# Kernel tuning notes

Measured on AMD Instinct MI355X. Metric: run time of the kernel, lower is better.

Reference implementation:

```python
import jax, jax.numpy as jnp
import numpy as np

N_NODES = 100000
N_EDGES = 800000
D = 128
BN_EPS = 1e-5


def setup_inputs() -> dict:
    key = jax.random.key(0)
    k1, k2, k3 = jax.random.split(key, 3)
    x = jax.random.normal(k1, (N_NODES, D), dtype=jnp.float32)
    # Glorot-ish init for the GCN weight
    W = jax.random.normal(k2, (D, D), dtype=jnp.float32) * (1.0 / np.sqrt(D))
    b = jnp.zeros((D,), dtype=jnp.float32)
    gamma = jnp.ones((D,), dtype=jnp.float32)
    beta = jnp.zeros((D,), dtype=jnp.float32)
    edge_index = jax.random.randint(k3, (2, N_EDGES), 0, N_NODES, dtype=jnp.int64)
    return {"x": x, "W": W, "b": b, "gamma": gamma, "beta": beta,
            "edge_index": edge_index}


def reference(x, W, b, gamma, beta, edge_index):
    N = x.shape[0]
    # --- GCNConv: add self-loops, symmetric degree normalization ---
    loop = jnp.arange(N, dtype=edge_index.dtype)
    src = jnp.concatenate([edge_index[0], loop])
    dst = jnp.concatenate([edge_index[1], loop])
    deg = jax.ops.segment_sum(jnp.ones_like(dst, dtype=x.dtype), dst,
                              num_segments=N)
    deg_inv_sqrt = jax.lax.rsqrt(deg)  # deg >= 1 thanks to self-loops
    norm = deg_inv_sqrt[src] * deg_inv_sqrt[dst]  # [E+N]

    h = x @ W  # [N, D] linear transform before propagation
    msg = h[src] * norm[:, None]  # gather + edge scaling, [E+N, D]
    agg = jax.ops.segment_sum(msg, dst, num_segments=N) + b  # scatter-add

    # --- BatchNorm1d (training-mode batch statistics, biased variance) ---
    mean = jnp.mean(agg, axis=0)
    var = jnp.mean(jnp.square(agg - mean), axis=0)
    y = gamma * (agg - mean) * jax.lax.rsqrt(var + BN_EPS) + beta

    # --- ReLU (dropout is identity in deterministic reference) ---
    return jax.nn.relu(y)
```

## Files before the change

kernel.cpp:

```cpp
#include <hip/hip_runtime.h>


#define N_NODES 100000
#define N_EDGES 800000
#define D 128
#define BN_EPS 1e-5f
#define SCAN_NB 98

__global__ void detect_i64(const unsigned int* ei, int* flag) {
    __shared__ int nonzero;
    if (threadIdx.x == 0) nonzero = 0;
    __syncthreads();
    int local = 0;
    for (int i = threadIdx.x; i < 2048; i += 256)
        if (ei[2 * i + 1] != 0u) local = 1;
    if (local) atomicOr(&nonzero, 1);
    __syncthreads();
    if (threadIdx.x == 0) *flag = (nonzero == 0) ? 1 : 0;
}

__device__ __forceinline__ int edge_at(const void* ei, int is64, long long pos) {
    if (is64) return (int)((const long long*)ei)[pos];
    return ((const int*)ei)[pos];
}

__global__ void count_deg_i(const void* ei, const int* __restrict__ flag,
                            int* __restrict__ deg) {
    int is64 = *flag;
    for (int i = blockIdx.x * blockDim.x + threadIdx.x; i < N_EDGES;
         i += gridDim.x * blockDim.x) {
        int d = edge_at(ei, is64, (long long)N_EDGES + i);
        atomicAdd(&deg[d], 1);
    }
}

__global__ __launch_bounds__(256) void scan1(const int* __restrict__ deg,
                                             int* __restrict__ rp,
                                             int* __restrict__ bsum) {
    __shared__ int wsum[4];
    int tid = threadIdx.x;
    int base = blockIdx.x * 1024;
    int v[4];
#pragma unroll
    for (int i = 0; i < 4; ++i) {
        int idx = base + tid * 4 + i;
        v[i] = (idx < N_NODES) ? deg[idx] : 0;
    }
    int tsum = v[0] + v[1] + v[2] + v[3];
    int lane = tid & 63;
    int incl = tsum;
#pragma unroll
    for (int off = 1; off < 64; off <<= 1) {
        int n = __shfl_up(incl, off, 64);
        if (lane >= off) incl += n;
    }
    int wid = tid >> 6;
    if (lane == 63) wsum[wid] = incl;
    __syncthreads();
    int woff = 0;
    for (int w = 0; w < wid; ++w) woff += wsum[w];
    int run = woff + incl - tsum;
#pragma unroll
    for (int i = 0; i < 4; ++i) {
        int idx = base + tid * 4 + i;
        if (idx < N_NODES) rp[idx] = run;
        run += v[i];
    }
    if (tid == 255) bsum[blockIdx.x] = woff + incl;
}

__global__ void scan2(int* __restrict__ bsum, int* __restrict__ rp) {
    __shared__ int s[128];
    int t = threadIdx.x;
    if (t < SCAN_NB) s[t] = bsum[t];
    __syncthreads();
    if (t == 0) {
        int run = 0;
        for (int i = 0; i < SCAN_NB; ++i) { int x = s[i]; s[i] = run; run += x; }
        rp[N_NODES] = N_EDGES;
    }
    __syncthreads();
    if (t < SCAN_NB) bsum[t] = s[t];
}

__global__ void scan3(int* __restrict__ rp, const int* __restrict__ bsum,
                      int* __restrict__ fp, const int* __restrict__ deg,
                      float* __restrict__ dis) {
    int idx = blockIdx.x * 256 + threadIdx.x;
    if (idx < N_NODES) {
        int v = rp[idx] + bsum[idx >> 10];
        rp[idx] = v;
        fp[idx] = v;
        dis[idx] = rsqrtf((float)deg[idx] + 1.0f);
    }
}

__global__ void fill_csr(const void* ei, const int* __restrict__ flag,
                         int* __restrict__ fp, const float* __restrict__ dis,
                         int2* __restrict__ eb) {
    int is64 = *flag;
    for (int e = blockIdx.x * blockDim.x + threadIdx.x; e < N_EDGES;
         e += gridDim.x * blockDim.x) {
        int s = edge_at(ei, is64, e);
        int d = edge_at(ei, is64, (long long)N_EDGES + e);
        float coef = dis[s] * dis[d];
        int pos = atomicAdd(&fp[d], 1);
        eb[pos] = make_int2(s, __float_as_int(coef));
    }
}

__global__ __launch_bounds__(256) void gather_x(const int* __restrict__ rp,
                                                const int2* __restrict__ eb,
                                                const float* __restrict__ dis,
                                                const float* __restrict__ x,
                                                float* __restrict__ aggx) {
    int lane = threadIdx.x & 63;
    int wid = threadIdx.x >> 6;
    const float2* x2 = (const float2*)x;
    for (int node = blockIdx.x * 4 + wid; node < N_NODES;
         node += gridDim.x * 4) {
        int beg = rp[node], end = rp[node + 1];
        float dd = dis[node];
        float2 xv = x2[(size_t)node * 64 + lane];
        float c2 = dd * dd;
        float a0 = xv.x * c2, a1 = xv.y * c2;
        int j = beg;
        for (; j + 4 <= end; j += 4) {
            int2 e0 = eb[j], e1 = eb[j + 1], e2 = eb[j + 2], e3 = eb[j + 3];
            float2 v0 = x2[(size_t)e0.x * 64 + lane];
            float2 v1 = x2[(size_t)e1.x * 64 + lane];
            float2 v2 = x2[(size_t)e2.x * 64 + lane];
            float2 v3 = x2[(size_t)e3.x * 64 + lane];
            float c0 = __int_as_float(e0.y), c1 = __int_as_float(e1.y);
            float cc = __int_as_float(e2.y), c3 = __int_as_float(e3.y);
            a0 = fmaf(v0.x, c0, a0); a1 = fmaf(v0.y, c0, a1);
            a0 = fmaf(v1.x, c1, a0); a1 = fmaf(v1.y, c1, a1);
            a0 = fmaf(v2.x, cc, a0); a1 = fmaf(v2.y, cc, a1);
            a0 = fmaf(v3.x, c3, a0); a1 = fmaf(v3.y, c3, a1);
        }
        for (; j < end; ++j) {
            int2 e = eb[j];
            float2 v = x2[(size_t)e.x * 64 + lane];
            float c = __int_as_float(e.y);
            a0 = fmaf(v.x, c, a0); a1 = fmaf(v.y, c, a1);
        }
        ((float2*)aggx)[(size_t)node * 64 + lane] = make_float2(a0, a1);
    }
}

__global__ __launch_bounds__(256) void gemm_stats(float* __restrict__ ax,
                                                  const float* __restrict__ Wm,
                                                  float* __restrict__ colsum,
                                                  float* __restrict__ colsumsq) {
    __shared__ float red[8 * 128];
    int tid = threadIdx.x;
    int row0 = blockIdx.x * 64;
    int tx = tid & 31;
    int ty = tid >> 5;

    const float4* W4 = (const float4*)Wm;

    const float4* arow[8];
    float rmask[8];
#pragma unroll
    for (int r = 0; r < 8; ++r) {
        int gr = row0 + ty * 8 + r;
        int cg = (gr < N_NODES) ? gr : 0;
        arow[r] = (const float4*)(ax + (size_t)cg * 128);
        rmask[r] = (gr < N_NODES) ? 1.0f : 0.0f;
    }

    float acc[8][4] = {};

    for (int kc = 0; kc < 32; ++kc) {
        float4 a8[8];
#pragma unroll
        for (int r = 0; r < 8; ++r) a8[r] = arow[r][kc];
        float4 w[4];
#pragma unroll
        for (int kk = 0; kk < 4; ++kk) w[kk] = W4[(kc * 4 + kk) * 32 + tx];
#pragma unroll
        for (int kk = 0; kk < 4; ++kk) {
#pragma unroll
            for (int r = 0; r < 8; ++r) {
                float av = (kk == 0) ? a8[r].x : (kk == 1) ? a8[r].y
                         : (kk == 2) ? a8[r].z : a8[r].w;
                acc[r][0] = fmaf(av, w[kk].x, acc[r][0]);
                acc[r][1] = fmaf(av, w[kk].y, acc[r][1]);
                acc[r][2] = fmaf(av, w[kk].z, acc[r][2]);
                acc[r][3] = fmaf(av, w[kk].w, acc[r][3]);
            }
        }
    }

#pragma unroll
    for (int r = 0; r < 8; ++r) {
        int gr = row0 + ty * 8 + r;
        if (gr < N_NODES)
            ((float4*)&ax[(size_t)gr * 128])[tx] =
                make_float4(acc[r][0], acc[r][1], acc[r][2], acc[r][3]);
    }

    float ps[4] = {0.f, 0.f, 0.f, 0.f}, pq[4] = {0.f, 0.f, 0.f, 0.f};
#pragma unroll
    for (int r = 0; r < 8; ++r)
#pragma unroll
        for (int k = 0; k < 4; ++k) {
            float v = acc[r][k] * rmask[r];
            ps[k] += v;
            pq[k] += v * v;
        }
#pragma unroll
    for (int k = 0; k < 4; ++k) {
        ps[k] += __shfl_xor(ps[k], 32);
        pq[k] += __shfl_xor(pq[k], 32);
    }
    int wv = tid >> 6;
    if ((tid & 32) == 0) {
#pragma unroll
        for (int k = 0; k < 4; ++k) {
            red[wv * 128 + tx * 4 + k] = ps[k];
            red[(4 + wv) * 128 + tx * 4 + k] = pq[k];
        }
    }
    __syncthreads();
    if (tid < 128) {
        float s = 0.f, q = 0.f;
#pragma unroll
        for (int w = 0; w < 4; ++w) {
            s += red[w * 128 + tid];
            q += red[(4 + w) * 128 + tid];
        }
        atomicAdd(&colsum[tid], s);
        atomicAdd(&colsumsq[tid], q);
    }
}

__global__ void finalize_bn(const float* __restrict__ colsum,
                            const float* __restrict__ colsumsq,
                            const float* __restrict__ gamma,
                            const float* __restrict__ beta,
                            float* __restrict__ scale, float* __restrict__ shift) {
    int c = threadIdx.x;
    float mean = colsum[c] * (1.0f / N_NODES);
    float var = colsumsq[c] * (1.0f / N_NODES) - mean * mean;
    float sc = gamma[c] * rsqrtf(var + BN_EPS);
    scale[c] = sc;
    shift[c] = beta[c] - mean * sc;
}

__global__ __launch_bounds__(256) void normalize_relu(float* __restrict__ out,
                                                      const float* __restrict__ scale,
                                                      const float* __restrict__ shift) {
    const int total = N_NODES * 32;
    float4* o4 = (float4*)out;
    const float4* sc4 = (const float4*)scale;
    const float4* sh4 = (const float4*)shift;
    for (int i = blockIdx.x * blockDim.x + threadIdx.x; i < total;
         i += gridDim.x * blockDim.x) {
        int cg = i & 31;
        float4 v = o4[i];
        float4 sc = sc4[cg];
        float4 sh = sh4[cg];
        v.x = fmaxf(fmaf(v.x, sc.x, sh.x), 0.f);
        v.y = fmaxf(fmaf(v.y, sc.y, sh.y), 0.f);
        v.z = fmaxf(fmaf(v.z, sc.z, sh.z), 0.f);
        v.w = fmaxf(fmaf(v.w, sc.w, sh.w), 0.f);
        o4[i] = v;
    }
}

extern "C" void kernel_launch(void* const* d_in, const int* in_sizes, int n_in,
                              void* d_out, int out_size, void* d_ws, size_t ws_size,
                              hipStream_t stream) {
    const float* x = (const float*)d_in[0];
    const float* Wm = (const float*)d_in[1];
    const float* gamma = (const float*)d_in[3];
    const float* beta = (const float*)d_in[4];
    const void* ei = d_in[5];

    float* out = (float*)d_out;

    int2* eb = (int2*)d_ws;
    int* deg = (int*)(eb + N_EDGES);
    int* rp = deg + N_NODES;
    int* fp = rp + N_NODES + 1;
    int* bsum = fp + N_NODES;
    float* dis = (float*)(bsum + 128);
    float* colsum = dis + N_NODES;
    float* colsumsq = colsum + 128;
    float* scale = colsumsq + 128;
    float* shift = scale + 128;
    int* flag = (int*)(shift + 128);

    hipMemsetAsync(deg, 0, (size_t)N_NODES * sizeof(int), stream);
    hipMemsetAsync(colsum, 0, 256 * sizeof(float), stream);

    detect_i64<<<1, 256, 0, stream>>>((const unsigned int*)ei, flag);
    count_deg_i<<<2048, 256, 0, stream>>>(ei, flag, deg);
    scan1<<<SCAN_NB, 256, 0, stream>>>(deg, rp, bsum);
    scan2<<<1, 128, 0, stream>>>(bsum, rp);
    scan3<<<(N_NODES + 255) / 256, 256, 0, stream>>>(rp, bsum, fp, deg, dis);
    fill_csr<<<2048, 256, 0, stream>>>(ei, flag, fp, dis, eb);
    gather_x<<<2048, 256, 0, stream>>>(rp, eb, dis, x, out);
    gemm_stats<<<(N_NODES + 63) / 64, 256, 0, stream>>>(out, Wm, colsum, colsumsq);
    finalize_bn<<<1, 128, 0, stream>>>(colsum, colsumsq, gamma, beta, scale, shift);
    normalize_relu<<<2048, 256, 0, stream>>>(out, scale, shift);
}
```

Measured before the change: 400.3 us.

## Stage GEMM tiles into LDS with async global_load_lds double buffering

```diff
diff --git a/kernel.cpp b/kernel.cpp
--- a/kernel.cpp
+++ b/kernel.cpp
@@ -6,6 +6,13 @@
 #define D 128
 #define BN_EPS 1e-5f
 #define SCAN_NB 98
+
+typedef const __attribute__((address_space(1))) void* gas_ptr;
+typedef __attribute__((address_space(3))) void* las_ptr;
+
+__device__ __forceinline__ void gload16(const float* g, void* l) {
+    __builtin_amdgcn_global_load_lds((gas_ptr)(const void*)g, (las_ptr)l, 16, 0, 0);
+}
 
 __global__ void detect_i64(const unsigned int* ei, int* flag) {
     __shared__ int nonzero;
@@ -152,45 +159,66 @@
                                                   const float* __restrict__ Wm,
                                                   float* __restrict__ colsum,
                                                   float* __restrict__ colsumsq) {
-    __shared__ float red[8 * 128];
+    __shared__ float Abuf[2][64 * 32];
+    __shared__ float Wbuf[2][32 * 128];
     int tid = threadIdx.x;
-    int row0 = blockIdx.x * 64;
     int tx = tid & 31;
     int ty = tid >> 5;
-
-    const float4* W4 = (const float4*)Wm;
-
-    const float4* arow[8];
-    float rmask[8];
-#pragma unroll
-    for (int r = 0; r < 8; ++r) {
-        int gr = row0 + ty * 8 + r;
-        int cg = (gr < N_NODES) ? gr : 0;
-        arow[r] = (const float4*)(ax + (size_t)cg * 128);
-        rmask[r] = (gr < N_NODES) ? 1.0f : 0.0f;
-    }
+    int wid = tid >> 6;
+    int lane = tid & 63;
+    int row0 = blockIdx.x * 64;
+
+    auto stage = [&](int b, int kc) {
+#pragma unroll
+        for (int i = 0; i < 2; ++i) {
+            int seg = wid * 2 + i;
+            int idx = seg * 64 + lane;
+            int row = idx >> 3, c4 = idx & 7;
+            int gr = row0 + row;
+            if (gr >= N_NODES) gr = N_NODES - 1;
+            const float* src = ax + (size_t)gr * 128 + kc + c4 * 4;
+            gload16(src, (char*)&Abuf[b][0] + seg * 1024);
+        }
+#pragma unroll
+        for (int i = 0; i < 4; ++i) {
+            int seg = wid * 4 + i;
+            int idx = seg * 64 + lane;
+            const float* src = Wm + (size_t)kc * 128 + (size_t)idx * 4;
+            gload16(src, (char*)&Wbuf[b][0] + seg * 1024);
+        }
+    };
+
+    stage(0, 0);
+    __syncthreads();
 
     float acc[8][4] = {};
 
-    for (int kc = 0; kc < 32; ++kc) {
-        float4 a8[8];
-#pragma unroll
-        for (int r = 0; r < 8; ++r) a8[r] = arow[r][kc];
-        float4 w[4];
-#pragma unroll
-        for (int kk = 0; kk < 4; ++kk) w[kk] = W4[(kc * 4 + kk) * 32 + tx];
-#pragma unroll
-        for (int kk = 0; kk < 4; ++kk) {
-#pragma unroll
-            for (int r = 0; r < 8; ++r) {
-                float av = (kk == 0) ? a8[r].x : (kk == 1) ? a8[r].y
-                         : (kk == 2) ? a8[r].z : a8[r].w;
-                acc[r][0] = fmaf(av, w[kk].x, acc[r][0]);
-                acc[r][1] = fmaf(av, w[kk].y, acc[r][1]);
-                acc[r][2] = fmaf(av, w[kk].z, acc[r][2]);
-                acc[r][3] = fmaf(av, w[kk].w, acc[r][3]);
+#pragma unroll 1
+    for (int t = 0; t < 4; ++t) {
+        if (t < 3) stage((t + 1) & 1, (t + 1) * 32);
+        asm volatile("" ::: "memory");
+        const float4* As4 = (const float4*)Abuf[t & 1];
+        const float4* Ws4 = (const float4*)Wbuf[t & 1];
+        for (int k4 = 0; k4 < 32; k4 += 4) {
+            float4 a8[8];
+#pragma unroll
+            for (int r = 0; r < 8; ++r)
+                a8[r] = As4[(ty * 8 + r) * 8 + (k4 >> 2)];
+#pragma unroll
+            for (int kk = 0; kk < 4; ++kk) {
+                float4 w = Ws4[(k4 + kk) * 32 + tx];
+#pragma unroll
+                for (int r = 0; r < 8; ++r) {
+                    float av = (kk == 0) ? a8[r].x : (kk == 1) ? a8[r].y
+                             : (kk == 2) ? a8[r].z : a8[r].w;
+                    acc[r][0] = fmaf(av, w.x, acc[r][0]);
+                    acc[r][1] = fmaf(av, w.y, acc[r][1]);
+                    acc[r][2] = fmaf(av, w.z, acc[r][2]);
+                    acc[r][3] = fmaf(av, w.w, acc[r][3]);
+                }
             }
         }
+        __syncthreads();
     }
 
 #pragma unroll
@@ -203,24 +231,27 @@
 
     float ps[4] = {0.f, 0.f, 0.f, 0.f}, pq[4] = {0.f, 0.f, 0.f, 0.f};
 #pragma unroll
-    for (int r = 0; r < 8; ++r)
+    for (int r = 0; r < 8; ++r) {
+        int gr = row0 + ty * 8 + r;
+        float m = (gr < N_NODES) ? 1.0f : 0.0f;
 #pragma unroll
         for (int k = 0; k < 4; ++k) {
-            float v = acc[r][k] * rmask[r];
+            float v = acc[r][k] * m;
             ps[k] += v;
             pq[k] += v * v;
         }
+    }
 #pragma unroll
     for (int k = 0; k < 4; ++k) {
         ps[k] += __shfl_xor(ps[k], 32);
         pq[k] += __shfl_xor(pq[k], 32);
     }
-    int wv = tid >> 6;
+    float* red = (float*)Abuf;
     if ((tid & 32) == 0) {
 #pragma unroll
         for (int k = 0; k < 4; ++k) {
-            red[wv * 128 + tx * 4 + k] = ps[k];
-            red[(4 + wv) * 128 + tx * 4 + k] = pq[k];
+            red[wid * 128 + tx * 4 + k] = ps[k];
+            red[1024 + wid * 128 + tx * 4 + k] = pq[k];
         }
     }
     __syncthreads();
@@ -229,7 +260,7 @@
 #pragma unroll
         for (int w = 0; w < 4; ++w) {
             s += red[w * 128 + tid];
-            q += red[(4 + w) * 128 + tid];
+            q += red[1024 + w * 128 + tid];
         }
         atomicAdd(&colsum[tid], s);
         atomicAdd(&colsumsq[tid], q);
```

After: 355.8 us. -11.1%, faster.

## Replace FP32 FMA GEMM with split-bf16 MFMA GEMM fused with column stats

Applied to the files above, without the earlier changes.

```diff
diff --git a/kernel.cpp b/kernel.cpp
--- a/kernel.cpp
+++ b/kernel.cpp
@@ -6,6 +6,18 @@
 #define D 128
 #define BN_EPS 1e-5f
 #define SCAN_NB 98
+
+using bf16x8 = __attribute__((ext_vector_type(8))) short;
+using f32x4 = __attribute__((ext_vector_type(4))) float;
+
+__device__ __forceinline__ unsigned short f2b(float f) {
+    unsigned u = __float_as_uint(f);
+    unsigned r = ((u >> 16) & 1u) + 0x7fffu;
+    return (unsigned short)((u + r) >> 16);
+}
+__device__ __forceinline__ float b2f(unsigned short h) {
+    return __uint_as_float(((unsigned)h) << 16);
+}
 
 __global__ void detect_i64(const unsigned int* ei, int* flag) {
     __shared__ int nonzero;
@@ -109,11 +121,33 @@
     }
 }
 
+__global__ void prep_w(const float* __restrict__ Wm, bf16x8* __restrict__ Whi,
+                       bf16x8* __restrict__ Wlo) {
+    for (int slot = threadIdx.x; slot < 2048; slot += 256) {
+        int t = slot >> 9;
+        int rem = slot & 511;
+        int c = rem >> 6;
+        int l = rem & 63;
+        int k0 = t * 32 + ((l >> 4) << 3);
+        int col = c * 16 + (l & 15);
+        bf16x8 hi, lo;
+#pragma unroll
+        for (int j = 0; j < 8; ++j) {
+            float v = Wm[(size_t)(k0 + j) * 128 + col];
+            unsigned short h = f2b(v);
+            hi[j] = (short)h;
+            lo[j] = (short)f2b(v - b2f(h));
+        }
+        Whi[slot] = hi;
+        Wlo[slot] = lo;
+    }
+}
+
 __global__ __launch_bounds__(256) void gather_x(const int* __restrict__ rp,
                                                 const int2* __restrict__ eb,
                                                 const float* __restrict__ dis,
                                                 const float* __restrict__ x,
-                                                float* __restrict__ aggx) {
+                                                void* __restrict__ aggx) {
     int lane = threadIdx.x & 63;
     int wid = threadIdx.x >> 6;
     const float2* x2 = (const float2*)x;
@@ -144,93 +178,68 @@
             float c = __int_as_float(e.y);
             a0 = fmaf(v.x, c, a0); a1 = fmaf(v.y, c, a1);
         }
-        ((float2*)aggx)[(size_t)node * 64 + lane] = make_float2(a0, a1);
-    }
-}
-
-__global__ __launch_bounds__(256) void gemm_stats(float* __restrict__ ax,
-                                                  const float* __restrict__ Wm,
-                                                  float* __restrict__ colsum,
-                                                  float* __restrict__ colsumsq) {
-    __shared__ float red[8 * 128];
+        unsigned short h0 = f2b(a0), h1 = f2b(a1);
+        unsigned short q0 = f2b(a0 - b2f(h0)), q1 = f2b(a1 - b2f(h1));
+        ushort2* rowp = (ushort2*)((char*)aggx + (size_t)node * 512);
+        rowp[lane] = make_ushort2(h0, h1);
+        rowp[64 + lane] = make_ushort2(q0, q1);
+    }
+}
+
+__global__ __launch_bounds__(256) void gemm_mfma(float* __restrict__ out,
+                                                 const bf16x8* __restrict__ Whi,
+                                                 const bf16x8* __restrict__ Wlo,
+                                                 float* __restrict__ colsum,
+                                                 float* __restrict__ colsumsq) {
+    __shared__ float sps[4][128], spq[4][128];
     int tid = threadIdx.x;
+    int w = tid >> 6;
+    int l = tid & 63;
     int row0 = blockIdx.x * 64;
-    int tx = tid & 31;
-    int ty = tid >> 5;
-
-    const float4* W4 = (const float4*)Wm;
-
-    const float4* arow[8];
-    float rmask[8];
-#pragma unroll
-    for (int r = 0; r < 8; ++r) {
-        int gr = row0 + ty * 8 + r;
-        int cg = (gr < N_NODES) ? gr : 0;
-        arow[r] = (const float4*)(ax + (size_t)cg * 128);
-        rmask[r] = (gr < N_NODES) ? 1.0f : 0.0f;
-    }
-
-    float acc[8][4] = {};
-
-    for (int kc = 0; kc < 32; ++kc) {
-        float4 a8[8];
-#pragma unroll
-        for (int r = 0; r < 8; ++r) a8[r] = arow[r][kc];
-        float4 w[4];
-#pragma unroll
-        for (int kk = 0; kk < 4; ++kk) w[kk] = W4[(kc * 4 + kk) * 32 + tx];
-#pragma unroll
-        for (int kk = 0; kk < 4; ++kk) {
-#pragma unroll
-            for (int r = 0; r < 8; ++r) {
-                float av = (kk == 0) ? a8[r].x : (kk == 1) ? a8[r].y
-                         : (kk == 2) ? a8[r].z : a8[r].w;
-                acc[r][0] = fmaf(av, w[kk].x, acc[r][0]);
-                acc[r][1] = fmaf(av, w[kk].y, acc[r][1]);
-                acc[r][2] = fmaf(av, w[kk].z, acc[r][2]);
-                acc[r][3] = fmaf(av, w[kk].w, acc[r][3]);
+
+    int arow = row0 + w * 16 + (l & 15);
+    if (arow >= N_NODES) arow = N_NODES - 1;
+    const char* abase = (const char*)out + (size_t)arow * 512;
+    int ao = (l >> 4) << 4;
+    bf16x8 ahi[4], alo[4];
+#pragma unroll
+    for (int t = 0; t < 4; ++t) {
+        ahi[t] = *(const bf16x8*)(abase + t * 64 + ao);
+        alo[t] = *(const bf16x8*)(abase + 256 + t * 64 + ao);
+    }
+
+    int rbase = row0 + w * 16 + ((l >> 4) << 2);
+#pragma unroll
+    for (int c = 0; c < 8; ++c) {
+        f32x4 acc = {0.f, 0.f, 0.f, 0.f};
+#pragma unroll
+        for (int t = 0; t < 4; ++t) {
+            bf16x8 bh = Whi[(t * 8 + c) * 64 + l];
+            bf16x8 bl = Wlo[(t * 8 + c) * 64 + l];
+            acc = __builtin_amdgcn_mfma_f32_16x16x32_bf16(ahi[t], bh, acc, 0, 0, 0);
+            acc = __builtin_amdgcn_mfma_f32_16x16x32_bf16(alo[t], bh, acc, 0, 0, 0);
+            acc = __builtin_amdgcn_mfma_f32_16x16x32_bf16(ahi[t], bl, acc, 0, 0, 0);
+        }
+        int col = c * 16 + (l & 15);
+        float ps = 0.f, pq = 0.f;
+#pragma unroll
+        for (int j = 0; j < 4; ++j) {
+            int orow = rbase + j;
+            float v = acc[j];
+            if (orow < N_NODES) {
+                out[(size_t)orow * 128 + col] = v;
+                ps += v;
+                pq += v * v;
             }
         }
-    }
-
-#pragma unroll
-    for (int r = 0; r < 8; ++r) {
-        int gr = row0 + ty * 8 + r;
-        if (gr < N_NODES)
-            ((float4*)&ax[(size_t)gr * 128])[tx] =
-                make_float4(acc[r][0], acc[r][1], acc[r][2], acc[r][3]);
-    }
-
-    float ps[4] = {0.f, 0.f, 0.f, 0.f}, pq[4] = {0.f, 0.f, 0.f, 0.f};
-#pragma unroll
-    for (int r = 0; r < 8; ++r)
-#pragma unroll
-        for (int k = 0; k < 4; ++k) {
-            float v = acc[r][k] * rmask[r];
-            ps[k] += v;
-            pq[k] += v * v;
-        }
-#pragma unroll
-    for (int k = 0; k < 4; ++k) {
-        ps[k] += __shfl_xor(ps[k], 32);
-        pq[k] += __shfl_xor(pq[k], 32);
-    }
-    int wv = tid >> 6;
-    if ((tid & 32) == 0) {
-#pragma unroll
-        for (int k = 0; k < 4; ++k) {
-            red[wv * 128 + tx * 4 + k] = ps[k];
-            red[(4 + wv) * 128 + tx * 4 + k] = pq[k];
-        }
+        ps += __shfl_xor(ps, 16); pq += __shfl_xor(pq, 16);
+        ps += __shfl_xor(ps, 32); pq += __shfl_xor(pq, 32);
+        if (l < 16) { sps[w][c * 16 + l] = ps; spq[w][c * 16 + l] = pq; }
     }
     __syncthreads();
     if (tid < 128) {
-        float s = 0.f, q = 0.f;
-#pragma unroll
-        for (int w = 0; w < 4; ++w) {
-            s += red[w * 128 + tid];
-            q += red[(4 + w) * 128 + tid];
-        }
+        float s = sps[0][tid] + sps[1][tid] + sps[2][tid] + sps[3][tid];
+        float q = spq[0][tid] + spq[1][tid] + spq[2][tid] + spq[3][tid];
         atomicAdd(&colsum[tid], s);
         atomicAdd(&colsumsq[tid], q);
     }
@@ -282,7 +291,9 @@
     float* out = (float*)d_out;
 
     int2* eb = (int2*)d_ws;
-    int* deg = (int*)(eb + N_EDGES);
+    bf16x8* Whi = (bf16x8*)(eb + N_EDGES);
+    bf16x8* Wlo = Whi + 2048;
+    int* deg = (int*)(Wlo + 2048);
     int* rp = deg + N_NODES;
     int* fp = rp + N_NODES + 1;
     int* bsum = fp + N_NODES;
@@ -302,8 +313,10 @@
     scan2<<<1, 128, 0, stream>>>(bsum, rp);
     scan3<<<(N_NODES + 255) / 256, 256, 0, stream>>>(rp, bsum, fp, deg, dis);
     fill_csr<<<2048, 256, 0, stream>>>(ei, flag, fp, dis, eb);
-    gather_x<<<2048, 256, 0, stream>>>(rp, eb, dis, x, out);
-    gemm_stats<<<(N_NODES + 63) / 64, 256, 0, stream>>>(out, Wm, colsum, colsumsq);
+    prep_w<<<1, 256, 0, stream>>>(Wm, Whi, Wlo);
+    gather_x<<<2048, 256, 0, stream>>>(rp, eb, dis, x, d_out);
+    gemm_mfma<<<(N_NODES + 63) / 64, 256, 0, stream>>>(out, Whi, Wlo, colsum,
+                                                       colsumsq);
     finalize_bn<<<1, 128, 0, stream>>>(colsum, colsumsq, gamma, beta, scale, shift);
     normalize_relu<<<2048, 256, 0, stream>>>(out, scale, shift);
 }
```

After: 358.5 us. 1.12x faster.
